# Optimization experiments

Measured on AMD Instinct MI355X. Metric: run time of the kernel, lower is better.

## Reference

```python
import jax, jax.numpy as jnp
import numpy as np

N_NODES = 100000
N_EDGES = 1600000
D = 128  # node_feat_size == edge_hidden_size


def setup_inputs() -> dict:
    key = jax.random.key(0)
    ks = jax.random.split(key, 10)
    s = 1.0 / np.sqrt(D)
    return {
        "node_feats": jax.random.normal(ks[0], (N_NODES, D), jnp.float32),
        "edge_logits": jax.random.normal(ks[1], (N_EDGES, 1), jnp.float32),
        "W_proj": jax.random.normal(ks[2], (D, D), jnp.float32) * s,
        "b_proj": jax.random.normal(ks[3], (D,), jnp.float32) * s,
        "W1": jax.random.normal(ks[4], (2 * D, D), jnp.float32) * s,
        "b1": jax.random.normal(ks[5], (D,), jnp.float32) * s,
        "W2": jax.random.normal(ks[6], (D, D), jnp.float32) * s,
        "b2": jax.random.normal(ks[7], (D,), jnp.float32) * s,
        "src": jax.random.randint(ks[8], (N_EDGES,), 0, N_NODES),
        "dst": jax.random.randint(ks[9], (N_EDGES,), 0, N_NODES),
    }


def reference(node_feats, edge_logits, W_proj, b_proj, W1, b1, W2, b2, src, dst):
    # ---- edge_softmax: softmax of edge_logits grouped by destination node ----
    # [E,1] logits; per-dst max for numerical stability (gradient-free shift)
    m = jax.ops.segment_max(edge_logits, dst, num_segments=N_NODES)  # [N,1]
    m = jnp.where(jnp.isfinite(m), m, 0.0)  # nodes with no in-edges
    e = jnp.exp(edge_logits - jax.lax.stop_gradient(m)[dst])  # [E,1]
    z = jax.ops.segment_sum(e, dst, num_segments=N_NODES)  # [N,1]
    a = e / z[dst]  # [E,1]

    # ---- project_node (dropout is identity at inference) ----
    hv = node_feats @ W_proj + b_proj  # [N,D]

    # ---- src_mul_edge + sum aggregation: c[v] = sum_{(u->v)} a_uv * hv[u] ----
    msg = hv[src] * a  # [E,D]
    c = jax.ops.segment_sum(msg, dst, num_segments=N_NODES)  # [N,D]

    context = jax.nn.elu(c)
    x = jnp.concatenate([context, node_feats], axis=1)  # [N,2D]
    h = jax.nn.relu(x @ W1 + b1)  # Linear -> Dropout(id) -> ReLU
    out = jax.nn.relu(h @ W2 + b2)  # Linear -> Dropout(id), outer ReLU
    return out
```

## Files before the change

### kernel.cpp

```cpp
#include <hip/hip_runtime.h>
#include <hip/hip_bf16.h>

typedef __hip_bfloat16 bf16;
typedef __attribute__((ext_vector_type(8))) __bf16 bf16x8;
typedef __attribute__((ext_vector_type(4))) float floatx4;

#define BUCKET_SHIFT 7
#define BUCKET_NODES 128
#define MAX_NB 1024

__device__ __forceinline__ unsigned short f2b(float f) {
    bf16 h = __float2bfloat16(f);
    unsigned short s;
    __builtin_memcpy(&s, &h, 2);
    return s;
}
__device__ __forceinline__ float b2f(unsigned short u) {
    unsigned int x = ((unsigned int)u) << 16;
    float f;
    __builtin_memcpy(&f, &x, 4);
    return f;
}
__device__ __forceinline__ float load_dual(const void* p, long long i, bool isbf) {
    return isbf ? b2f(((const unsigned short*)p)[i]) : ((const float*)p)[i];
}
__device__ __forceinline__ bf16x8 ldsfrag(const unsigned short* p) {
    union { uint4 u; bf16x8 v; } t;
    t.u = *(const uint4*)p;
    return t.v;
}

__global__ __launch_bounds__(64) void detect_kernel(const unsigned int* __restrict__ words,
                                                    int* __restrict__ flag) {
    int cnt = 0;
    for (int i = threadIdx.x; i < 4096; i += 64) {
        unsigned int lo = words[i] & 0xFFFFu;
        unsigned int e = (lo >> 7) & 0xFFu;
        if (lo == 0u || (e >= 110u && e <= 135u)) cnt++;
    }
#pragma unroll
    for (int off = 32; off > 0; off >>= 1) cnt += __shfl_down(cnt, off, 64);
    if (threadIdx.x == 0) *flag = (cnt > 2458) ? 1 : 0;
}

__global__ __launch_bounds__(256) void transpose_w_kernel(const void* __restrict__ W,
                                                          unsigned short* __restrict__ Wt,
                                                          const int* __restrict__ flag, int K) {
    bool isbf = (*flag != 0);
    int idx = blockIdx.x * 256 + threadIdx.x;
    if (idx >= 128 * K) return;
    int n = idx / K, k = idx - n * K;
    Wt[idx] = f2b(load_dual(W, (long long)k * 128 + n, isbf));
}

__global__ __launch_bounds__(256) void bhist_kernel(const int* __restrict__ dst,
                                                    int* __restrict__ bcount, int E) {
    __shared__ int lcnt[MAX_NB];
    for (int i = threadIdx.x; i < MAX_NB; i += 256) lcnt[i] = 0;
    __syncthreads();
    int base = blockIdx.x * 8192;
#pragma unroll
    for (int j = 0; j < 32; ++j) {
        int e = base + j * 256 + threadIdx.x;
        if (e < E) atomicAdd(&lcnt[dst[e] >> BUCKET_SHIFT], 1);
    }
    __syncthreads();
    for (int i = threadIdx.x; i < MAX_NB; i += 256)
        if (lcnt[i]) atomicAdd(&bcount[i], lcnt[i]);
}

__global__ __launch_bounds__(256) void bscan_kernel(const int* __restrict__ bcount,
                                                    int* __restrict__ bstart,
                                                    int* __restrict__ bcursor, int NB) {
    int t = threadIdx.x;
    int v[4];
    int sum = 0;
#pragma unroll
    for (int j = 0; j < 4; ++j) {
        int i = t * 4 + j;
        v[j] = (i < NB) ? bcount[i] : 0;
        sum += v[j];
    }
    int lane = t & 63, wave = t >> 6;
    int inc = sum;
#pragma unroll
    for (int off = 1; off < 64; off <<= 1) {
        int x = __shfl_up(inc, off, 64);
        if (lane >= off) inc += x;
    }
    __shared__ int wsum[4];
    if (lane == 63) wsum[wave] = inc;
    __syncthreads();
    int woff = 0;
    for (int w = 0; w < wave; ++w) woff += wsum[w];
    int run = inc - sum + woff;
#pragma unroll
    for (int j = 0; j < 4; ++j) {
        int i = t * 4 + j;
        if (i < NB) { bstart[i] = run; bcursor[i] = run; }
        run += v[j];
    }
}

__global__ __launch_bounds__(256) void bappend_kernel(const int* __restrict__ dst,
                                                      const int* __restrict__ src,
                                                      const void* __restrict__ logits,
                                                      int* __restrict__ bcursor,
                                                      uint2* __restrict__ ebuf,
                                                      const int* __restrict__ flag, int E) {
    __shared__ int lcnt[MAX_NB];
    __shared__ int lbase[MAX_NB];
    for (int i = threadIdx.x; i < MAX_NB; i += 256) lcnt[i] = 0;
    __syncthreads();
    const bool isbf = (*flag != 0);
    int base = blockIdx.x * 8192;
#pragma unroll
    for (int j = 0; j < 32; ++j) {
        int e = base + j * 256 + threadIdx.x;
        if (e < E) atomicAdd(&lcnt[dst[e] >> BUCKET_SHIFT], 1);
    }
    __syncthreads();
    for (int i = threadIdx.x; i < MAX_NB; i += 256) {
        int c = lcnt[i];
        if (c) { lbase[i] = atomicAdd(&bcursor[i], c); lcnt[i] = 0; }
    }
    __syncthreads();
#pragma unroll
    for (int j = 0; j < 32; ++j) {
        int e = base + j * 256 + threadIdx.x;
        if (e < E) {
            int d = dst[e];
            int b = d >> BUCKET_SHIFT;
            float w = expf(load_dual(logits, e, isbf));
            int pos = lbase[b] + atomicAdd(&lcnt[b], 1);
            uint2 rec;
            rec.x = (unsigned int)src[e] | ((unsigned int)(d & (BUCKET_NODES - 1)) << 24);
            rec.y = __float_as_uint(w);
            ebuf[pos] = rec;
        }
    }
}

__global__ __launch_bounds__(256) void bcsr_kernel(const uint2* __restrict__ ebuf,
                                                   const int* __restrict__ bstart,
                                                   const int* __restrict__ bcount,
                                                   uint2* __restrict__ ebuf2,
                                                   int* __restrict__ row_start,
                                                   int* __restrict__ ncount, int N) {
    __shared__ int lcnt[BUCKET_NODES];
    __shared__ int lbase[BUCKET_NODES];
    const int b = blockIdx.x;
    const int s0 = bstart[b];
    const int cnt = bcount[b];
    if (threadIdx.x < BUCKET_NODES) lcnt[threadIdx.x] = 0;
    __syncthreads();
    for (int i = threadIdx.x; i < cnt; i += 256)
        atomicAdd(&lcnt[ebuf[s0 + i].x >> 24], 1);
    __syncthreads();
    if (threadIdx.x < 64) {
        int lane = threadIdx.x;
        int carry = 0;
#pragma unroll
        for (int half = 0; half < 2; ++half) {
            int idx = half * 64 + lane;
            int v = lcnt[idx];
            int inc = v;
#pragma unroll
            for (int off = 1; off < 64; off <<= 1) {
                int t = __shfl_up(inc, off, 64);
                if (lane >= off) inc += t;
            }
            lbase[idx] = carry + inc - v;
            carry += __shfl(inc, 63, 64);
        }
    }
    __syncthreads();
    if (threadIdx.x < BUCKET_NODES) {
        int gn = b * BUCKET_NODES + threadIdx.x;
        if (gn < N) {
            row_start[gn] = s0 + lbase[threadIdx.x];
            ncount[gn] = lcnt[threadIdx.x];
        }
    }
    __syncthreads();
    if (threadIdx.x < BUCKET_NODES) lcnt[threadIdx.x] = 0;
    __syncthreads();
    for (int i = threadIdx.x; i < cnt; i += 256) {
        uint2 rec = ebuf[s0 + i];
        int dl = rec.x >> 24;
        int pos = lbase[dl] + atomicAdd(&lcnt[dl], 1);
        ebuf2[s0 + pos] = make_uint2(rec.x & 0xFFFFFFu, rec.y);
    }
}

__global__ __launch_bounds__(256) void agg_csr_kernel(const int* __restrict__ row_start,
                                                      const int* __restrict__ ncount,
                                                      const uint2* __restrict__ erec,
                                                      const unsigned int* __restrict__ hv32,
                                                      unsigned int* __restrict__ ctx32, int N) {
    int n = blockIdx.x * 4 + (threadIdx.x >> 6);
    int lane = threadIdx.x & 63;
    if (n >= N) return;
    int s0 = row_start[n];
    int deg = ncount[n];
    float accx = 0.f, accy = 0.f, z = 0.f;
    int i = 0;
    for (; i + 8 <= deg; i += 8) {
        uint2 r[8];
        unsigned int h[8];
#pragma unroll
        for (int j = 0; j < 8; ++j) r[j] = erec[s0 + i + j];
#pragma unroll
        for (int j = 0; j < 8; ++j) h[j] = hv32[(size_t)r[j].x * 64 + lane];
#pragma unroll
        for (int j = 0; j < 8; ++j) {
            float w = __uint_as_float(r[j].y);
            z += w;
            accx += w * b2f((unsigned short)h[j]);
            accy += w * b2f((unsigned short)(h[j] >> 16));
        }
    }
    for (; i + 4 <= deg; i += 4) {
        uint2 r[4];
        unsigned int h[4];
#pragma unroll
        for (int j = 0; j < 4; ++j) r[j] = erec[s0 + i + j];
#pragma unroll
        for (int j = 0; j < 4; ++j) h[j] = hv32[(size_t)r[j].x * 64 + lane];
#pragma unroll
        for (int j = 0; j < 4; ++j) {
            float w = __uint_as_float(r[j].y);
            z += w;
            accx += w * b2f((unsigned short)h[j]);
            accy += w * b2f((unsigned short)(h[j] >> 16));
        }
    }
    for (; i < deg; ++i) {
        uint2 r = erec[s0 + i];
        unsigned int h = hv32[(size_t)r.x * 64 + lane];
        float w = __uint_as_float(r.y);
        z += w;
        accx += w * b2f((unsigned short)h);
        accy += w * b2f((unsigned short)(h >> 16));
    }
    float rz = (z > 0.f) ? 1.f / z : 0.f;
    float x = accx * rz, y = accy * rz;
    x = x > 0.f ? x : expm1f(x);
    y = y > 0.f ? y : expm1f(y);
    ctx32[(size_t)n * 64 + lane] = ((unsigned int)f2b(y) << 16) | f2b(x);
}

template <int K, int MODE, bool RELU, bool A_DUAL, bool OUT_DUAL>
__global__ __launch_bounds__(256) void gemm_mfma(const void* __restrict__ A,
                                                 const unsigned short* __restrict__ Actx,
                                                 const unsigned short* __restrict__ Wt,
                                                 const void* __restrict__ bias,
                                                 void* __restrict__ outp,
                                                 const int* __restrict__ flag, int N) {
    __shared__ unsigned short Alds[128 * 72];
    __shared__ unsigned short Wlds[128 * 72];
    const bool isbf = (*flag != 0);
    const int t = threadIdx.x;
    const int wid = t >> 6;
    const int lane = t & 63;
    const int m16 = lane & 15;
    const int quad = lane >> 4;
    const int row0 = blockIdx.x * 128;

    floatx4 acc[2][8];
#pragma unroll
    for (int i = 0; i < 2; ++i)
#pragma unroll
        for (int j = 0; j < 8; ++j) acc[i][j] = (floatx4){0.f, 0.f, 0.f, 0.f};

    const int r  = t >> 1;
    const int kh = (t & 1) * 32;

#pragma unroll
    for (int kc = 0; kc < K / 64; ++kc) {
        {
            const unsigned short* wp = Wt + (size_t)r * K + kc * 64 + kh;
            uint4* o = (uint4*)&Wlds[r * 72 + kh];
            o[0] = ((const uint4*)wp)[0];
            o[1] = ((const uint4*)wp)[1];
            o[2] = ((const uint4*)wp)[2];
            o[3] = ((const uint4*)wp)[3];
        }
        {
            int grow = row0 + r;
            if (grow >= N) grow = N - 1;
            uint4* o = (uint4*)&Alds[r * 72 + kh];
            if (MODE == 1 && kc < 2) {
                const unsigned short* ap = Actx + (size_t)grow * 128 + kc * 64 + kh;
                o[0] = ((const uint4*)ap)[0];
                o[1] = ((const uint4*)ap)[1];
                o[2] = ((const uint4*)ap)[2];
                o[3] = ((const uint4*)ap)[3];
            } else {
                const int stride = (MODE == 1) ? 128 : K;
                const int kabs = (MODE == 1) ? (kc * 64 - 128 + kh) : (kc * 64 + kh);
                if (A_DUAL && !isbf) {
                    const float* ap = (const float*)A + (size_t)grow * stride + kabs;
#pragma unroll
                    for (int q = 0; q < 4; ++q) {
                        float4 v0 = ((const float4*)ap)[2 * q];
                        float4 v1 = ((const float4*)ap)[2 * q + 1];
                        union { uint4 u; unsigned short s[8]; } P;
                        P.s[0] = f2b(v0.x); P.s[1] = f2b(v0.y);
                        P.s[2] = f2b(v0.z); P.s[3] = f2b(v0.w);
                        P.s[4] = f2b(v1.x); P.s[5] = f2b(v1.y);
                        P.s[6] = f2b(v1.z); P.s[7] = f2b(v1.w);
                        o[q] = P.u;
                    }
                } else {
                    const unsigned short* ap = (const unsigned short*)A + (size_t)grow * stride + kabs;
                    o[0] = ((const uint4*)ap)[0];
                    o[1] = ((const uint4*)ap)[1];
                    o[2] = ((const uint4*)ap)[2];
                    o[3] = ((const uint4*)ap)[3];
                }
            }
        }
        __syncthreads();

#pragma unroll
        for (int c = 0; c < 2; ++c) {
            const int ko = c * 32 + quad * 8;
            bf16x8 a0 = ldsfrag(&Alds[(wid * 32 + m16) * 72 + ko]);
            bf16x8 a1 = ldsfrag(&Alds[(wid * 32 + 16 + m16) * 72 + ko]);
#pragma unroll
            for (int nt = 0; nt < 8; ++nt) {
                bf16x8 bb = ldsfrag(&Wlds[(nt * 16 + m16) * 72 + ko]);
                acc[0][nt] = __builtin_amdgcn_mfma_f32_16x16x32_bf16(a0, bb, acc[0][nt], 0, 0, 0);
                acc[1][nt] = __builtin_amdgcn_mfma_f32_16x16x32_bf16(a1, bb, acc[1][nt], 0, 0, 0);
            }
        }
        __syncthreads();
    }

#pragma unroll
    for (int mt = 0; mt < 2; ++mt) {
        int gr0 = row0 + wid * 32 + mt * 16 + quad * 4;
#pragma unroll
        for (int nt = 0; nt < 8; ++nt) {
            int col = nt * 16 + m16;
            float bb = load_dual(bias, col, isbf);
#pragma unroll
            for (int rg = 0; rg < 4; ++rg) {
                int gr = gr0 + rg;
                if (gr < N) {
                    float x = acc[mt][nt][rg] + bb;
                    if (RELU) x = x > 0.f ? x : 0.f;
                    if (OUT_DUAL && !isbf)
                        ((float*)outp)[(size_t)gr * 128 + col] = x;
                    else
                        ((unsigned short*)outp)[(size_t)gr * 128 + col] = f2b(x);
                }
            }
        }
    }
}

extern "C" void kernel_launch(void* const* d_in, const int* in_sizes, int n_in,
                              void* d_out, int out_size, void* d_ws, size_t ws_size,
                              hipStream_t stream) {
    const void* node_feats  = d_in[0];
    const void* edge_logits = d_in[1];
    const void* W_proj      = d_in[2];
    const void* b_proj      = d_in[3];
    const void* W1          = d_in[4];
    const void* b1          = d_in[5];
    const void* W2          = d_in[6];
    const void* b2          = d_in[7];
    const int*  src         = (const int*)d_in[8];
    const int*  dst         = (const int*)d_in[9];

    const int N = in_sizes[0] / 128;
    const int E = in_sizes[8];
    const int NB = (N + BUCKET_NODES - 1) / BUCKET_NODES;

    char* ws = (char*)d_ws;
    size_t off = 0;
    unsigned short* hv    = (unsigned short*)(ws + off); off += (size_t)N * 256;
    unsigned short* ctx   = (unsigned short*)(ws + off); off += (size_t)N * 256;
    unsigned short* h_buf = (unsigned short*)(ws + off); off += (size_t)N * 256;
    uint2* ebuf  = (uint2*)(ws + off); off += (size_t)E * 8;
    uint2* ebuf2 = (uint2*)(ws + off); off += (size_t)E * 8;
    unsigned short* Wtp = (unsigned short*)(ws + off); off += 128 * 128 * 2;
    unsigned short* Wt1 = (unsigned short*)(ws + off); off += 128 * 256 * 2;
    unsigned short* Wt2 = (unsigned short*)(ws + off); off += 128 * 128 * 2;
    int* bcount    = (int*)(ws + off); off += MAX_NB * 4;
    int* bstart    = (int*)(ws + off); off += MAX_NB * 4;
    int* bcursor   = (int*)(ws + off); off += MAX_NB * 4;
    int* row_start = (int*)(ws + off); off += (size_t)N * 4;
    int* ncount    = (int*)(ws + off); off += (size_t)N * 4;
    int* flag      = (int*)(ws + off);

    const int gblocks = (N + 127) / 128;
    const int ebblocks = (E + 8191) / 8192;

    detect_kernel<<<1, 64, 0, stream>>>((const unsigned int*)node_feats, flag);
    hipMemsetAsync(bcount, 0, MAX_NB * 4, stream);

    transpose_w_kernel<<<(128 * 128 + 255) / 256, 256, 0, stream>>>(W_proj, Wtp, flag, 128);
    transpose_w_kernel<<<(128 * 256 + 255) / 256, 256, 0, stream>>>(W1, Wt1, flag, 256);
    transpose_w_kernel<<<(128 * 128 + 255) / 256, 256, 0, stream>>>(W2, Wt2, flag, 128);

    bhist_kernel<<<ebblocks, 256, 0, stream>>>(dst, bcount, E);
    bscan_kernel<<<1, 256, 0, stream>>>(bcount, bstart, bcursor, NB);
    bappend_kernel<<<ebblocks, 256, 0, stream>>>(dst, src, edge_logits, bcursor,
                                                 ebuf, flag, E);
    bcsr_kernel<<<NB, 256, 0, stream>>>(ebuf, bstart, bcount, ebuf2,
                                        row_start, ncount, N);

    gemm_mfma<128, 0, false, true, false><<<gblocks, 256, 0, stream>>>(
        node_feats, nullptr, Wtp, b_proj, hv, flag, N);

    agg_csr_kernel<<<(N + 3) / 4, 256, 0, stream>>>(row_start, ncount, ebuf2,
                                                    (const unsigned int*)hv,
                                                    (unsigned int*)ctx, N);

    gemm_mfma<256, 1, true, true, false><<<gblocks, 256, 0, stream>>>(
        node_feats, ctx, Wt1, b1, h_buf, flag, N);
    gemm_mfma<128, 0, true, false, true><<<gblocks, 256, 0, stream>>>(
        h_buf, nullptr, Wt2, b2, d_out, flag, N);
}
```

Baseline: 381.1 us.

## Fuse MLP GEMMs into one kernel and load A fragments directly from global

Merges the two MLP linear layers into a single kernel. The ReLU'd hidden activations stay in per-wave LDS instead of round-tripping through a global bf16 buffer. The projection and first-layer GEMMs now load A operand fragments straight from global memory into registers rather than staging them in LDS, and the three weight-transpose launches are combined into one. This removes one kernel launch and roughly 50 MB of intermediate global traffic, at the cost of more LDS per block and uncoalesced-ish per-lane row fragment loads.

```diff
diff --git a/kernel.cpp b/kernel.cpp
--- a/kernel.cpp
+++ b/kernel.cpp
@@ -27,6 +27,20 @@
 __device__ __forceinline__ bf16x8 ldsfrag(const unsigned short* p) {
     union { uint4 u; bf16x8 v; } t;
     t.u = *(const uint4*)p;
+    return t.v;
+}
+__device__ __forceinline__ bf16x8 gfrag_dual(const void* A, int row, int stride, int k0, bool isbf) {
+    if (isbf) {
+        union { uint4 u; bf16x8 v; } t;
+        t.u = *(const uint4*)((const unsigned short*)A + (size_t)row * stride + k0);
+        return t.v;
+    }
+    const float* ap = (const float*)A + (size_t)row * stride + k0;
+    float4 v0 = ((const float4*)ap)[0];
+    float4 v1 = ((const float4*)ap)[1];
+    union { unsigned short s[8]; bf16x8 v; } t;
+    t.s[0] = f2b(v0.x); t.s[1] = f2b(v0.y); t.s[2] = f2b(v0.z); t.s[3] = f2b(v0.w);
+    t.s[4] = f2b(v1.x); t.s[5] = f2b(v1.y); t.s[6] = f2b(v1.z); t.s[7] = f2b(v1.w);
     return t.v;
 }
 
@@ -43,14 +57,27 @@
     if (threadIdx.x == 0) *flag = (cnt > 2458) ? 1 : 0;
 }
 
-__global__ __launch_bounds__(256) void transpose_w_kernel(const void* __restrict__ W,
-                                                          unsigned short* __restrict__ Wt,
-                                                          const int* __restrict__ flag, int K) {
+__global__ __launch_bounds__(256) void transpose_all_kernel(const void* __restrict__ Wp,
+                                                            const void* __restrict__ W1,
+                                                            const void* __restrict__ W2,
+                                                            unsigned short* __restrict__ Wtp,
+                                                            unsigned short* __restrict__ Wt1,
+                                                            unsigned short* __restrict__ Wt2,
+                                                            const int* __restrict__ flag) {
     bool isbf = (*flag != 0);
     int idx = blockIdx.x * 256 + threadIdx.x;
-    if (idx >= 128 * K) return;
-    int n = idx / K, k = idx - n * K;
-    Wt[idx] = f2b(load_dual(W, (long long)k * 128 + n, isbf));
+    if (idx < 16384) {
+        int n = idx >> 7, k = idx & 127;
+        Wtp[idx] = f2b(load_dual(Wp, (long long)k * 128 + n, isbf));
+    } else if (idx < 49152) {
+        int j = idx - 16384;
+        int n = j >> 8, k = j & 255;
+        Wt1[j] = f2b(load_dual(W1, (long long)k * 128 + n, isbf));
+    } else if (idx < 65536) {
+        int j = idx - 49152;
+        int n = j >> 7, k = j & 127;
+        Wt2[j] = f2b(load_dual(W2, (long long)k * 128 + n, isbf));
+    }
 }
 
 __global__ __launch_bounds__(256) void bhist_kernel(const int* __restrict__ dst,
@@ -250,22 +277,24 @@
     ctx32[(size_t)n * 64 + lane] = ((unsigned int)f2b(y) << 16) | f2b(x);
 }
 
-template <int K, int MODE, bool RELU, bool A_DUAL, bool OUT_DUAL>
-__global__ __launch_bounds__(256) void gemm_mfma(const void* __restrict__ A,
-                                                 const unsigned short* __restrict__ Actx,
+__global__ __launch_bounds__(256) void gemm_proj(const void* __restrict__ A,
                                                  const unsigned short* __restrict__ Wt,
                                                  const void* __restrict__ bias,
-                                                 void* __restrict__ outp,
+                                                 unsigned short* __restrict__ hv,
                                                  const int* __restrict__ flag, int N) {
-    __shared__ unsigned short Alds[128 * 72];
-    __shared__ unsigned short Wlds[128 * 72];
+    __shared__ unsigned short Wl[128 * 136];
     const bool isbf = (*flag != 0);
-    const int t = threadIdx.x;
-    const int wid = t >> 6;
-    const int lane = t & 63;
-    const int m16 = lane & 15;
-    const int quad = lane >> 4;
+    const int t = threadIdx.x, wid = t >> 6, lane = t & 63;
+    const int m16 = lane & 15, quad = lane >> 4;
     const int row0 = blockIdx.x * 128;
+    {
+        int r = t >> 1, kh = (t & 1) * 64;
+        const uint4* s = (const uint4*)(Wt + (size_t)r * 128 + kh);
+        uint4* d = (uint4*)&Wl[r * 136 + kh];
+#pragma unroll
+        for (int q = 0; q < 8; ++q) d[q] = s[q];
+    }
+    __syncthreads();
 
     floatx4 acc[2][8];
 #pragma unroll
@@ -273,69 +302,20 @@
 #pragma unroll
         for (int j = 0; j < 8; ++j) acc[i][j] = (floatx4){0.f, 0.f, 0.f, 0.f};
 
-    const int r  = t >> 1;
-    const int kh = (t & 1) * 32;
-
-#pragma unroll
-    for (int kc = 0; kc < K / 64; ++kc) {
-        {
-            const unsigned short* wp = Wt + (size_t)r * K + kc * 64 + kh;
-            uint4* o = (uint4*)&Wlds[r * 72 + kh];
-            o[0] = ((const uint4*)wp)[0];
-            o[1] = ((const uint4*)wp)[1];
-            o[2] = ((const uint4*)wp)[2];
-            o[3] = ((const uint4*)wp)[3];
-        }
-        {
-            int grow = row0 + r;
-            if (grow >= N) grow = N - 1;
-            uint4* o = (uint4*)&Alds[r * 72 + kh];
-            if (MODE == 1 && kc < 2) {
-                const unsigned short* ap = Actx + (size_t)grow * 128 + kc * 64 + kh;
-                o[0] = ((const uint4*)ap)[0];
-                o[1] = ((const uint4*)ap)[1];
-                o[2] = ((const uint4*)ap)[2];
-                o[3] = ((const uint4*)ap)[3];
-            } else {
-                const int stride = (MODE == 1) ? 128 : K;
-                const int kabs = (MODE == 1) ? (kc * 64 - 128 + kh) : (kc * 64 + kh);
-                if (A_DUAL && !isbf) {
-                    const float* ap = (const float*)A + (size_t)grow * stride + kabs;
-#pragma unroll
-                    for (int q = 0; q < 4; ++q) {
-                        float4 v0 = ((const float4*)ap)[2 * q];
-                        float4 v1 = ((const float4*)ap)[2 * q + 1];
-                        union { uint4 u; unsigned short s[8]; } P;
-                        P.s[0] = f2b(v0.x); P.s[1] = f2b(v0.y);
-                        P.s[2] = f2b(v0.z); P.s[3] = f2b(v0.w);
-                        P.s[4] = f2b(v1.x); P.s[5] = f2b(v1.y);
-                        P.s[6] = f2b(v1.z); P.s[7] = f2b(v1.w);
-                        o[q] = P.u;
-                    }
-                } else {
-                    const unsigned short* ap = (const unsigned short*)A + (size_t)grow * stride + kabs;
-                    o[0] = ((const uint4*)ap)[0];
-                    o[1] = ((const uint4*)ap)[1];
-                    o[2] = ((const uint4*)ap)[2];
-                    o[3] = ((const uint4*)ap)[3];
-                }
-            }
-        }
-        __syncthreads();
-
-#pragma unroll
-        for (int c = 0; c < 2; ++c) {
-            const int ko = c * 32 + quad * 8;
-            bf16x8 a0 = ldsfrag(&Alds[(wid * 32 + m16) * 72 + ko]);
-            bf16x8 a1 = ldsfrag(&Alds[(wid * 32 + 16 + m16) * 72 + ko]);
-#pragma unroll
-            for (int nt = 0; nt < 8; ++nt) {
-                bf16x8 bb = ldsfrag(&Wlds[(nt * 16 + m16) * 72 + ko]);
-                acc[0][nt] = __builtin_amdgcn_mfma_f32_16x16x32_bf16(a0, bb, acc[0][nt], 0, 0, 0);
-                acc[1][nt] = __builtin_amdgcn_mfma_f32_16x16x32_bf16(a1, bb, acc[1][nt], 0, 0, 0);
-            }
-        }
-        __syncthreads();
+    int ra0 = row0 + wid * 32 + m16;      if (ra0 >= N) ra0 = N - 1;
+    int ra1 = row0 + wid * 32 + 16 + m16; if (ra1 >= N) ra1 = N - 1;
+
+#pragma unroll
+    for (int c = 0; c < 4; ++c) {
+        int k0 = c * 32 + quad * 8;
+        bf16x8 a0 = gfrag_dual(A, ra0, 128, k0, isbf);
+        bf16x8 a1 = gfrag_dual(A, ra1, 128, k0, isbf);
+#pragma unroll
+        for (int nt = 0; nt < 8; ++nt) {
+            bf16x8 b = ldsfrag(&Wl[(nt * 16 + m16) * 136 + k0]);
+            acc[0][nt] = __builtin_amdgcn_mfma_f32_16x16x32_bf16(a0, b, acc[0][nt], 0, 0, 0);
+            acc[1][nt] = __builtin_amdgcn_mfma_f32_16x16x32_bf16(a1, b, acc[1][nt], 0, 0, 0);
+        }
     }
 
 #pragma unroll
@@ -345,16 +325,134 @@
         for (int nt = 0; nt < 8; ++nt) {
             int col = nt * 16 + m16;
             float bb = load_dual(bias, col, isbf);
+#pragma unroll
+            for (int rg = 0; rg < 4; ++rg) {
+                int gr = gr0 + rg;
+                if (gr < N) hv[(size_t)gr * 128 + col] = f2b(acc[mt][nt][rg] + bb);
+            }
+        }
+    }
+}
+
+__global__ __launch_bounds__(256) void mlp_fused(const unsigned short* __restrict__ ctx,
+                                                 const void* __restrict__ nf,
+                                                 const unsigned short* __restrict__ Wt1,
+                                                 const void* __restrict__ b1,
+                                                 const unsigned short* __restrict__ Wt2,
+                                                 const void* __restrict__ b2,
+                                                 void* __restrict__ outp,
+                                                 const int* __restrict__ flag, int N) {
+    __shared__ unsigned short Wl[128 * 72];
+    __shared__ unsigned short Hl[4][32 * 136];
+    const bool isbf = (*flag != 0);
+    const int t = threadIdx.x, wid = t >> 6, lane = t & 63;
+    const int m16 = lane & 15, quad = lane >> 4;
+    const int row0 = blockIdx.x * 128;
+
+    floatx4 acc[2][8];
+#pragma unroll
+    for (int i = 0; i < 2; ++i)
+#pragma unroll
+        for (int j = 0; j < 8; ++j) acc[i][j] = (floatx4){0.f, 0.f, 0.f, 0.f};
+
+    int ra0 = row0 + wid * 32 + m16;      if (ra0 >= N) ra0 = N - 1;
+    int ra1 = row0 + wid * 32 + 16 + m16; if (ra1 >= N) ra1 = N - 1;
+
+#pragma unroll
+    for (int kc = 0; kc < 4; ++kc) {
+        {
+            int r = t >> 1, kh = (t & 1) * 32;
+            const uint4* s = (const uint4*)(Wt1 + (size_t)r * 256 + kc * 64 + kh);
+            uint4* d = (uint4*)&Wl[r * 72 + kh];
+#pragma unroll
+            for (int q = 0; q < 4; ++q) d[q] = s[q];
+        }
+        __syncthreads();
+#pragma unroll
+        for (int c = 0; c < 2; ++c) {
+            int kl = c * 32 + quad * 8;
+            int ka = kc * 64 + kl;
+            bf16x8 a0, a1;
+            if (ka < 128) {
+                union { uint4 u; bf16x8 v; } t0, t1;
+                t0.u = *(const uint4*)(ctx + (size_t)ra0 * 128 + ka);
+                t1.u = *(const uint4*)(ctx + (size_t)ra1 * 128 + ka);
+                a0 = t0.v; a1 = t1.v;
+            } else {
+                a0 = gfrag_dual(nf, ra0, 128, ka - 128, isbf);
+                a1 = gfrag_dual(nf, ra1, 128, ka - 128, isbf);
+            }
+#pragma unroll
+            for (int nt = 0; nt < 8; ++nt) {
+                bf16x8 b = ldsfrag(&Wl[(nt * 16 + m16) * 72 + kl]);
+                acc[0][nt] = __builtin_amdgcn_mfma_f32_16x16x32_bf16(a0, b, acc[0][nt], 0, 0, 0);
+                acc[1][nt] = __builtin_amdgcn_mfma_f32_16x16x32_bf16(a1, b, acc[1][nt], 0, 0, 0);
+            }
+        }
+        __syncthreads();
+    }
+
+#pragma unroll
+    for (int nt = 0; nt < 8; ++nt) {
+        int col = nt * 16 + m16;
+        float bb = load_dual(b1, col, isbf);
+#pragma unroll
+        for (int mt = 0; mt < 2; ++mt) {
+#pragma unroll
+            for (int rg = 0; rg < 4; ++rg) {
+                int lr = mt * 16 + quad * 4 + rg;
+                float x = acc[mt][nt][rg] + bb;
+                Hl[wid][lr * 136 + col] = f2b(x > 0.f ? x : 0.f);
+            }
+        }
+    }
+
+#pragma unroll
+    for (int i = 0; i < 2; ++i)
+#pragma unroll
+        for (int j = 0; j < 8; ++j) acc[i][j] = (floatx4){0.f, 0.f, 0.f, 0.f};
+
+#pragma unroll
+    for (int kc = 0; kc < 2; ++kc) {
+        {
+            int r = t >> 1, kh = (t & 1) * 32;
+            const uint4* s = (const uint4*)(Wt2 + (size_t)r * 128 + kc * 64 + kh);
+            uint4* d = (uint4*)&Wl[r * 72 + kh];
+#pragma unroll
+            for (int q = 0; q < 4; ++q) d[q] = s[q];
+        }
+        __syncthreads();
+#pragma unroll
+        for (int c = 0; c < 2; ++c) {
+            int kl = c * 32 + quad * 8;
+            int ka = kc * 64 + kl;
+            bf16x8 a0 = ldsfrag(&Hl[wid][m16 * 136 + ka]);
+            bf16x8 a1 = ldsfrag(&Hl[wid][(16 + m16) * 136 + ka]);
+#pragma unroll
+            for (int nt = 0; nt < 8; ++nt) {
+                bf16x8 b = ldsfrag(&Wl[(nt * 16 + m16) * 72 + kl]);
+                acc[0][nt] = __builtin_amdgcn_mfma_f32_16x16x32_bf16(a0, b, acc[0][nt], 0, 0, 0);
+                acc[1][nt] = __builtin_amdgcn_mfma_f32_16x16x32_bf16(a1, b, acc[1][nt], 0, 0, 0);
+            }
+        }
+        __syncthreads();
+    }
+
+#pragma unroll
+    for (int mt = 0; mt < 2; ++mt) {
+        int gr0 = row0 + wid * 32 + mt * 16 + quad * 4;
+#pragma unroll
+        for (int nt = 0; nt < 8; ++nt) {
+            int col = nt * 16 + m16;
+            float bb = load_dual(b2, col, isbf);
 #pragma unroll
             for (int rg = 0; rg < 4; ++rg) {
                 int gr = gr0 + rg;
                 if (gr < N) {
                     float x = acc[mt][nt][rg] + bb;
-                    if (RELU) x = x > 0.f ? x : 0.f;
-                    if (OUT_DUAL && !isbf)
-                        ((float*)outp)[(size_t)gr * 128 + col] = x;
-                    else
-                        ((unsigned short*)outp)[(size_t)gr * 128 + col] = f2b(x);
+                    x = x > 0.f ? x : 0.f;
+                    if (!isbf) ((float*)outp)[(size_t)gr * 128 + col] = x;
+                    else       ((unsigned short*)outp)[(size_t)gr * 128 + col] = f2b(x);
                 }
             }
         }
@@ -381,9 +479,8 @@
 
     char* ws = (char*)d_ws;
     size_t off = 0;
-    unsigned short* hv    = (unsigned short*)(ws + off); off += (size_t)N * 256;
-    unsigned short* ctx   = (unsigned short*)(ws + off); off += (size_t)N * 256;
-    unsigned short* h_buf = (unsigned short*)(ws + off); off += (size_t)N * 256;
+    unsigned short* hv  = (unsigned short*)(ws + off); off += (size_t)N * 256;
+    unsigned short* ctx = (unsigned short*)(ws + off); off += (size_t)N * 256;
     uint2* ebuf  = (uint2*)(ws + off); off += (size_t)E * 8;
     uint2* ebuf2 = (uint2*)(ws + off); off += (size_t)E * 8;
     unsigned short* Wtp = (unsigned short*)(ws + off); off += 128 * 128 * 2;
@@ -402,9 +499,7 @@
     detect_kernel<<<1, 64, 0, stream>>>((const unsigned int*)node_feats, flag);
     hipMemsetAsync(bcount, 0, MAX_NB * 4, stream);
 
-    transpose_w_kernel<<<(128 * 128 + 255) / 256, 256, 0, stream>>>(W_proj, Wtp, flag, 128);
-    transpose_w_kernel<<<(128 * 256 + 255) / 256, 256, 0, stream>>>(W1, Wt1, flag, 256);
-    transpose_w_kernel<<<(128 * 128 + 255) / 256, 256, 0, stream>>>(W2, Wt2, flag, 128);
+    transpose_all_kernel<<<256, 256, 0, stream>>>(W_proj, W1, W2, Wtp, Wt1, Wt2, flag);
 
     bhist_kernel<<<ebblocks, 256, 0, stream>>>(dst, bcount, E);
     bscan_kernel<<<1, 256, 0, stream>>>(bcount, bstart, bcursor, NB);
@@ -413,15 +508,12 @@
     bcsr_kernel<<<NB, 256, 0, stream>>>(ebuf, bstart, bcount, ebuf2,
                                         row_start, ncount, N);
 
-    gemm_mfma<128, 0, false, true, false><<<gblocks, 256, 0, stream>>>(
-        node_feats, nullptr, Wtp, b_proj, hv, flag, N);
+    gemm_proj<<<gblocks, 256, 0, stream>>>(node_feats, Wtp, b_proj, hv, flag, N);
 
     agg_csr_kernel<<<(N + 3) / 4, 256, 0, stream>>>(row_start, ncount, ebuf2,
                                                     (const unsigned int*)hv,
                                                     (unsigned int*)ctx, N);
 
-    gemm_mfma<256, 1, true, true, false><<<gblocks, 256, 0, stream>>>(
-        node_feats, ctx, Wt1, b1, h_buf, flag, N);
-    gemm_mfma<128, 0, true, false, true><<<gblocks, 256, 0, stream>>>(
-        h_buf, nullptr, Wt2, b2, d_out, flag, N);
-}
+    mlp_fused<<<gblocks, 256, 0, stream>>>(ctx, node_feats, Wt1, b1, Wt2, b2,
+                                           d_out, flag, N);
+}
```

New measurement: 350.8 us. 7.9% less time.
